# Kernel optimization log

Measured on AMD Instinct MI355X. Metric: run time of the kernel, lower is better.

The kernel has to match this reference:

```python
import jax, jax.numpy as jnp
import numpy as np

B, CI, CO, F, H, W = 8, 32, 64, 4, 64, 64


def _grid(h, w):
    # channel 0 varies along W so dx = coords[0,1,0]-coords[0,0,0] is the uniform spacing
    xs = jnp.linspace(0.0, 1.0, w, dtype=jnp.float32)
    ys = jnp.linspace(0.0, 1.0, h, dtype=jnp.float32)
    gy, gx = jnp.meshgrid(ys, xs, indexing='ij')
    return jnp.stack([gx, gy], axis=-1)  # [h, w, 2]


def _trapz(x, dx, axis):
    # trapezoidal rule with uniform spacing dx along `axis`
    return dx * (x.sum(axis=axis) - 0.5 * (jnp.take(x, 0, axis=axis) + jnp.take(x, -1, axis=axis)))


def integral_2d(x, dx, dim1, dim2):
    # 2D quadrature over dims dim1 < dim2 (reduce dim2 first so dim1 index stays valid)
    return _trapz(_trapz(x, dx, dim2), dx, dim1)


def setup_inputs() -> dict:
    key = jax.random.key(0)
    k1, k2, k3 = jax.random.split(key, 3)
    fan_in_scale = 1.0 / np.sqrt(CI * 2)  # kaiming-ish init scale
    return {
        'v': jax.random.normal(k1, (B, CI, H, W), dtype=jnp.float32),
        'v_coords': _grid(H, W),
        'target_coords': _grid(H, W),
        'Wx': jax.random.normal(k2, (F, CO, CI, 2), dtype=jnp.float32) * fan_in_scale,
        'Wy': jax.random.normal(k3, (F, CO, CI, 2), dtype=jnp.float32) * fan_in_scale,
    }


def reference(v, v_coords, target_coords, Wx, Wy):
    # v: [b, i, h, w]; coords: [h, w, 2]; Wx/Wy: [f, o, i, 2]
    vp = jnp.transpose(v, (0, 2, 3, 1))                 # [b, h, w, i]
    dx = v_coords[0, 1, 0] - v_coords[0, 0, 0]
    iv = integral_2d(vp, dx, 1, 2)                      # [b, i]
    # == einsum('foid,hwd->hwfoi', Wx, target_coords) then 'hwfoi,bi->bhwfo'
    scaled = jnp.einsum('foid,bi,hwd->bhwfo', Wx, iv, target_coords, optimize=True)
    # == einsum('foid,hwd->hwfoi', Wy, v_coords) then 'hwfoi,bhwi->bhwfo'
    Wyvp = jnp.einsum('foid,hwd,bhwi->bhwfo', Wy, v_coords, vp, optimize=True)
    iw = integral_2d(Wyvp, dx, 1, 2)                    # [b, f, o]
    up = scaled + iw[:, None, None]                     # [b, h, w, f, o]
    up = up.sum(axis=3)                                 # [b, h, w, o]
    return jnp.transpose(up, (0, 3, 1, 2))              # [b, o, h, w]
```

## Files before the change

kernel.cpp:

```cpp
#include <hip/hip_runtime.h>

#define B_  8
#define CI_ 32
#define CO_ 64
#define F_  4
#define H_  64
#define W_  64

__global__ __launch_bounds__(1024) void k_fused(
    const float* __restrict__ v, const float* __restrict__ vc,
    const float* __restrict__ tc, const float* __restrict__ Wx,
    const float* __restrict__ Wy, float* __restrict__ out) {
  const int blk = blockIdx.x;
  const int b   = blk & 7;
  const int op  = blk >> 3;
  const int tid = threadIdx.x;

  __shared__ float4 wls[2][CI_];
  __shared__ float  red[16][8];
  __shared__ float  bc[2][4];

  if (tid < 2 * CI_) {
    const int i  = tid & (CI_ - 1);
    const int oo = tid >> 5;
    const int o  = op * 2 + oo;
    float wx0 = 0.f, wx1 = 0.f, wy0 = 0.f, wy1 = 0.f;
#pragma unroll
    for (int f = 0; f < F_; ++f) {
      const int base = ((f * CO_ + o) * CI_ + i) * 2;
      float2 wx = *(const float2*)(Wx + base);
      float2 wy = *(const float2*)(Wy + base);
      wx0 += wx.x; wx1 += wx.y; wy0 += wy.x; wy1 += wy.y;
    }
    wls[oo][i] = make_float4(wx0, wx1, wy0, wy1);
  }

  const int h  = tid >> 4;
  const int w4 = tid & 15;
#define GW_(w) ((((w) == 0) || ((w) == W_ - 1)) ? 0.5f : 1.0f)
  const int wsc = w4 * 4;
  const float wh = ((h == 0) || (h == H_ - 1)) ? 0.5f : 1.0f;
  const float4 wg = make_float4(wh * GW_(wsc), wh * GW_(wsc + 1),
                                wh * GW_(wsc + 2), wh * GW_(wsc + 3));
  const float cx0 = vc[2 * wsc],       cx1 = vc[2 * (wsc + 1)];
  const float cx2 = vc[2 * (wsc + 2)], cx3 = vc[2 * (wsc + 3)];
  const float cy  = vc[h * (W_ * 2) + 1];

  __syncthreads();

  float a00 = 0.f, a01 = 0.f, aC0 = 0.f;
  float a10 = 0.f, a11 = 0.f, aC1 = 0.f;
  const float4* vb = (const float4*)(v + (size_t)b * (CI_ * H_ * W_));
#pragma unroll 8
  for (int i = 0; i < CI_; ++i) {
    float4 a = vb[i * 1024 + tid];
    float t0 = a.x * wg.x, t1 = a.y * wg.y, t2 = a.z * wg.z, t3 = a.w * wg.w;
    float rs0 = (t0 + t1) + (t2 + t3);
    float rs1 = t0 * cx0 + t1 * cx1 + t2 * cx2 + t3 * cx3;
    float rs2 = cy * rs0;
    float4 wA = wls[0][i];
    float4 wB = wls[1][i];
    a00 += wA.x * rs0;  a01 += wA.y * rs0;  aC0 += wA.z * rs1 + wA.w * rs2;
    a10 += wB.x * rs0;  a11 += wB.y * rs0;  aC1 += wB.z * rs1 + wB.w * rs2;
  }

  for (int off = 32; off > 0; off >>= 1) {
    a00 += __shfl_down(a00, off, 64);
    a01 += __shfl_down(a01, off, 64);
    aC0 += __shfl_down(aC0, off, 64);
    a10 += __shfl_down(a10, off, 64);
    a11 += __shfl_down(a11, off, 64);
    aC1 += __shfl_down(aC1, off, 64);
  }
  const int wave = tid >> 6;
  if ((tid & 63) == 0) {
    red[wave][0] = a00; red[wave][1] = a01; red[wave][2] = aC0;
    red[wave][3] = a10; red[wave][4] = a11; red[wave][5] = aC1;
  }
  __syncthreads();
  if (tid < 16) {
    float r0 = red[tid][0], r1 = red[tid][1], r2 = red[tid][2];
    float r3 = red[tid][3], r4 = red[tid][4], r5 = red[tid][5];
    for (int off = 8; off > 0; off >>= 1) {
      r0 += __shfl_down(r0, off, 64);
      r1 += __shfl_down(r1, off, 64);
      r2 += __shfl_down(r2, off, 64);
      r3 += __shfl_down(r3, off, 64);
      r4 += __shfl_down(r4, off, 64);
      r5 += __shfl_down(r5, off, 64);
    }
    if (tid == 0) {
      const float dx = vc[2] - vc[0];
      const float sc = dx * dx;
      bc[0][0] = r0 * sc; bc[0][1] = r1 * sc; bc[0][2] = r2 * sc;
      bc[1][0] = r3 * sc; bc[1][1] = r4 * sc; bc[1][2] = r5 * sc;
    }
  }
  __syncthreads();

  const float4* tcp = (const float4*)(tc + (size_t)(h * W_ + wsc) * 2);
  const float4 t0v = tcp[0];
  const float4 t1v = tcp[1];

  {
    const float SX0 = bc[0][0], SX1 = bc[0][1], C = bc[0][2];
    float4 r;
    r.x = t0v.x * SX0 + t0v.y * SX1 + C;
    r.y = t0v.z * SX0 + t0v.w * SX1 + C;
    r.z = t1v.x * SX0 + t1v.y * SX1 + C;
    r.w = t1v.z * SX0 + t1v.w * SX1 + C;
    ((float4*)out)[(size_t)(b * CO_ + op * 2) * 1024 + tid] = r;
  }
  {
    const float SX0 = bc[1][0], SX1 = bc[1][1], C = bc[1][2];
    float4 r;
    r.x = t0v.x * SX0 + t0v.y * SX1 + C;
    r.y = t0v.z * SX0 + t0v.w * SX1 + C;
    r.z = t1v.x * SX0 + t1v.y * SX1 + C;
    r.w = t1v.z * SX0 + t1v.w * SX1 + C;
    ((float4*)out)[(size_t)(b * CO_ + op * 2 + 1) * 1024 + tid] = r;
  }
}

extern "C" void kernel_launch(void* const* d_in, const int* in_sizes, int n_in,
                              void* d_out, int out_size, void* d_ws, size_t ws_size,
                              hipStream_t stream) {
  const float* v  = (const float*)d_in[0];
  const float* vc = (const float*)d_in[1];
  const float* tc = (const float*)d_in[2];
  const float* Wx = (const float*)d_in[3];
  const float* Wy = (const float*)d_in[4];
  float* out = (float*)d_out;

  k_fused<<<B_ * (CO_ / 2), 1024, 0, stream>>>(v, vc, tc, Wx, Wy, out);
}
```

Before: 75.88 us.

## Split reduction across blocks with cooperative grid sync to avoid redundant input reads

Before, each of the 256 blocks read the whole 32-channel slice of v for its batch, so every input plane was re-read 32 times. Now each block reduces exactly one (b,i) plane into per-channel integrals stored in the workspace. After a cooperative grid-wide sync, each block combines the weights with those integrals and writes two output channels. This removes the redundant global reads but adds a grid barrier, a cooperative launch, and a round trip through global memory.

```diff
diff --git a/kernel.cpp b/kernel.cpp
--- a/kernel.cpp
+++ b/kernel.cpp
@@ -1,4 +1,7 @@
 #include <hip/hip_runtime.h>
+#include <hip/hip_cooperative_groups.h>
+
+namespace cg = cooperative_groups;
 
 #define B_  8
 #define CI_ 32
@@ -7,100 +10,108 @@
 #define H_  64
 #define W_  64
 
-__global__ __launch_bounds__(1024) void k_fused(
+__global__ __launch_bounds__(1024) void k_coop(
     const float* __restrict__ v, const float* __restrict__ vc,
     const float* __restrict__ tc, const float* __restrict__ Wx,
-    const float* __restrict__ Wy, float* __restrict__ out) {
+    const float* __restrict__ Wy, float* __restrict__ iv,
+    float* __restrict__ T, float* __restrict__ out) {
   const int blk = blockIdx.x;
-  const int b   = blk & 7;
-  const int op  = blk >> 3;
   const int tid = threadIdx.x;
 
-  __shared__ float4 wls[2][CI_];
-  __shared__ float  red[16][8];
-  __shared__ float  bc[2][4];
+  __shared__ float red[16][4];
+  __shared__ float red2[4][4];
+  __shared__ float bc[2][4];
 
-  if (tid < 2 * CI_) {
-    const int i  = tid & (CI_ - 1);
-    const int oo = tid >> 5;
+  const int h   = tid >> 4;
+  const int w4  = tid & 15;
+  const int wsc = w4 * 4;
+#define GW_(w) ((((w) == 0) || ((w) == W_ - 1)) ? 0.5f : 1.0f)
+  const float wh = ((h == 0) || (h == H_ - 1)) ? 0.5f : 1.0f;
+
+  const int b2 = blk >> 5;
+  const int op = blk & 31;
+  float2 wx2 = make_float2(0.f, 0.f), wy2 = make_float2(0.f, 0.f);
+  if (tid < 256) {
+    const int i  = tid & 31;
+    const int f  = (tid >> 5) & 3;
+    const int oo = tid >> 7;
     const int o  = op * 2 + oo;
-    float wx0 = 0.f, wx1 = 0.f, wy0 = 0.f, wy1 = 0.f;
-#pragma unroll
-    for (int f = 0; f < F_; ++f) {
-      const int base = ((f * CO_ + o) * CI_ + i) * 2;
-      float2 wx = *(const float2*)(Wx + base);
-      float2 wy = *(const float2*)(Wy + base);
-      wx0 += wx.x; wx1 += wx.y; wy0 += wy.x; wy1 += wy.y;
+    const int base = ((f * CO_ + o) * CI_ + i) * 2;
+    wx2 = *(const float2*)(Wx + base);
+    wy2 = *(const float2*)(Wy + base);
+  }
+  const float4* tcp = (const float4*)(tc + (size_t)(h * W_ + wsc) * 2);
+  const float4 t0v = tcp[0];
+  const float4 t1v = tcp[1];
+
+  {
+    const float4 wg = make_float4(GW_(wsc), GW_(wsc + 1),
+                                  GW_(wsc + 2), GW_(wsc + 3));
+    const float cx0 = vc[2 * wsc],       cx1 = vc[2 * (wsc + 1)];
+    const float cx2 = vc[2 * (wsc + 2)], cx3 = vc[2 * (wsc + 3)];
+    const float cy  = vc[h * (W_ * 2) + 1];
+
+    float4 a = ((const float4*)(v + (size_t)blk * (H_ * W_)))[tid];
+    float rs0 = a.x * wg.x + a.y * wg.y + a.z * wg.z + a.w * wg.w;
+    float rs1 = a.x * wg.x * cx0 + a.y * wg.y * cx1 +
+                a.z * wg.z * cx2 + a.w * wg.w * cx3;
+    float s0 = wh * rs0;
+    float s1 = wh * rs1;
+    float s2 = wh * cy * rs0;
+    for (int off = 32; off > 0; off >>= 1) {
+      s0 += __shfl_down(s0, off, 64);
+      s1 += __shfl_down(s1, off, 64);
+      s2 += __shfl_down(s2, off, 64);
     }
-    wls[oo][i] = make_float4(wx0, wx1, wy0, wy1);
+    const int wave = tid >> 6;
+    if ((tid & 63) == 0) {
+      red[wave][0] = s0; red[wave][1] = s1; red[wave][2] = s2;
+    }
+    __syncthreads();
+    if (tid < 16) {
+      float u0 = red[tid][0], u1 = red[tid][1], u2 = red[tid][2];
+      for (int off = 8; off > 0; off >>= 1) {
+        u0 += __shfl_down(u0, off, 64);
+        u1 += __shfl_down(u1, off, 64);
+        u2 += __shfl_down(u2, off, 64);
+      }
+      if (tid == 0) {
+        const float dx = vc[2] - vc[0];
+        const float sc = dx * dx;
+        iv[blk]        = u0 * sc;
+        T[2 * blk]     = u1 * sc;
+        T[2 * blk + 1] = u2 * sc;
+      }
+    }
   }
 
-  const int h  = tid >> 4;
-  const int w4 = tid & 15;
-#define GW_(w) ((((w) == 0) || ((w) == W_ - 1)) ? 0.5f : 1.0f)
-  const int wsc = w4 * 4;
-  const float wh = ((h == 0) || (h == H_ - 1)) ? 0.5f : 1.0f;
-  const float4 wg = make_float4(wh * GW_(wsc), wh * GW_(wsc + 1),
-                                wh * GW_(wsc + 2), wh * GW_(wsc + 3));
-  const float cx0 = vc[2 * wsc],       cx1 = vc[2 * (wsc + 1)];
-  const float cx2 = vc[2 * (wsc + 2)], cx3 = vc[2 * (wsc + 3)];
-  const float cy  = vc[h * (W_ * 2) + 1];
+  cg::this_grid().sync();
 
-  __syncthreads();
-
-  float a00 = 0.f, a01 = 0.f, aC0 = 0.f;
-  float a10 = 0.f, a11 = 0.f, aC1 = 0.f;
-  const float4* vb = (const float4*)(v + (size_t)b * (CI_ * H_ * W_));
-#pragma unroll 8
-  for (int i = 0; i < CI_; ++i) {
-    float4 a = vb[i * 1024 + tid];
-    float t0 = a.x * wg.x, t1 = a.y * wg.y, t2 = a.z * wg.z, t3 = a.w * wg.w;
-    float rs0 = (t0 + t1) + (t2 + t3);
-    float rs1 = t0 * cx0 + t1 * cx1 + t2 * cx2 + t3 * cx3;
-    float rs2 = cy * rs0;
-    float4 wA = wls[0][i];
-    float4 wB = wls[1][i];
-    a00 += wA.x * rs0;  a01 += wA.y * rs0;  aC0 += wA.z * rs1 + wA.w * rs2;
-    a10 += wB.x * rs0;  a11 += wB.y * rs0;  aC1 += wB.z * rs1 + wB.w * rs2;
-  }
-
-  for (int off = 32; off > 0; off >>= 1) {
-    a00 += __shfl_down(a00, off, 64);
-    a01 += __shfl_down(a01, off, 64);
-    aC0 += __shfl_down(aC0, off, 64);
-    a10 += __shfl_down(a10, off, 64);
-    a11 += __shfl_down(a11, off, 64);
-    aC1 += __shfl_down(aC1, off, 64);
-  }
-  const int wave = tid >> 6;
-  if ((tid & 63) == 0) {
-    red[wave][0] = a00; red[wave][1] = a01; red[wave][2] = aC0;
-    red[wave][3] = a10; red[wave][4] = a11; red[wave][5] = aC1;
-  }
-  __syncthreads();
-  if (tid < 16) {
-    float r0 = red[tid][0], r1 = red[tid][1], r2 = red[tid][2];
-    float r3 = red[tid][3], r4 = red[tid][4], r5 = red[tid][5];
-    for (int off = 8; off > 0; off >>= 1) {
-      r0 += __shfl_down(r0, off, 64);
-      r1 += __shfl_down(r1, off, 64);
-      r2 += __shfl_down(r2, off, 64);
-      r3 += __shfl_down(r3, off, 64);
-      r4 += __shfl_down(r4, off, 64);
-      r5 += __shfl_down(r5, off, 64);
+  if (tid < 256) {
+    const int i = tid & 31;
+    const float ivbi = iv[b2 * CI_ + i];
+    const float t0 = T[(b2 * CI_ + i) * 2];
+    const float t1 = T[(b2 * CI_ + i) * 2 + 1];
+    float sx0 = wx2.x * ivbi;
+    float sx1 = wx2.y * ivbi;
+    float c   = wy2.x * t0 + wy2.y * t1;
+    for (int off = 32; off > 0; off >>= 1) {
+      sx0 += __shfl_down(sx0, off, 64);
+      sx1 += __shfl_down(sx1, off, 64);
+      c   += __shfl_down(c,   off, 64);
     }
-    if (tid == 0) {
-      const float dx = vc[2] - vc[0];
-      const float sc = dx * dx;
-      bc[0][0] = r0 * sc; bc[0][1] = r1 * sc; bc[0][2] = r2 * sc;
-      bc[1][0] = r3 * sc; bc[1][1] = r4 * sc; bc[1][2] = r5 * sc;
+    if ((tid & 63) == 0) {
+      const int w = tid >> 6;
+      red2[w][0] = sx0; red2[w][1] = sx1; red2[w][2] = c;
     }
   }
   __syncthreads();
-
-  const float4* tcp = (const float4*)(tc + (size_t)(h * W_ + wsc) * 2);
-  const float4 t0v = tcp[0];
-  const float4 t1v = tcp[1];
+  if (tid < 2) {
+    bc[tid][0] = red2[2 * tid][0] + red2[2 * tid + 1][0];
+    bc[tid][1] = red2[2 * tid][1] + red2[2 * tid + 1][1];
+    bc[tid][2] = red2[2 * tid][2] + red2[2 * tid + 1][2];
+  }
+  __syncthreads();
 
   {
     const float SX0 = bc[0][0], SX1 = bc[0][1], C = bc[0][2];
@@ -109,7 +120,7 @@
     r.y = t0v.z * SX0 + t0v.w * SX1 + C;
     r.z = t1v.x * SX0 + t1v.y * SX1 + C;
     r.w = t1v.z * SX0 + t1v.w * SX1 + C;
-    ((float4*)out)[(size_t)(b * CO_ + op * 2) * 1024 + tid] = r;
+    ((float4*)out)[(size_t)(b2 * CO_ + op * 2) * 1024 + tid] = r;
   }
   {
     const float SX0 = bc[1][0], SX1 = bc[1][1], C = bc[1][2];
@@ -118,7 +129,7 @@
     r.y = t0v.z * SX0 + t0v.w * SX1 + C;
     r.z = t1v.x * SX0 + t1v.y * SX1 + C;
     r.w = t1v.z * SX0 + t1v.w * SX1 + C;
-    ((float4*)out)[(size_t)(b * CO_ + op * 2 + 1) * 1024 + tid] = r;
+    ((float4*)out)[(size_t)(b2 * CO_ + op * 2 + 1) * 1024 + tid] = r;
   }
 }
 
@@ -132,5 +143,11 @@
   const float* Wy = (const float*)d_in[4];
   float* out = (float*)d_out;
 
-  k_fused<<<B_ * (CO_ / 2), 1024, 0, stream>>>(v, vc, tc, Wx, Wy, out);
+  float* iv = (float*)d_ws;
+  float* T  = iv + B_ * CI_;
+
+  void* args[] = {(void*)&v, (void*)&vc, (void*)&tc, (void*)&Wx, (void*)&Wy,
+                  (void*)&iv, (void*)&T, (void*)&out};
+  hipLaunchCooperativeKernel((const void*)k_coop, dim3(B_ * CI_), dim3(1024),
+                             args, 0, stream);
 }
```

New measurement: 105.1 us. +38.5%, slower.
